# Performance work log

Measured on AMD Instinct MI355X. Metric: run time of the kernel, lower is better.

## Reference

```python
import jax, jax.numpy as jnp
import numpy as np

NPOINT = 10  # hardcoded in Sampler.__init__
INIT_DIST = 1e10  # matches pointnet2 CUDA kernel init


def setup_inputs() -> dict:
    key = jax.random.key(0)
    xyz = jax.random.normal(key, (64, 262144, 3), dtype=jnp.float32)
    return {"xyz": xyz}


def reference(xyz):
    """Furthest point sampling: returns (B, NPOINT) int32 indices,
    same semantics as pointnet2_utils.furthest_point_sample."""
    B, N, _ = xyz.shape
    init_dists = jnp.full((B, N), INIT_DIST, dtype=xyz.dtype)
    init_idx = jnp.zeros((B,), dtype=jnp.int32)  # kernel starts at index 0
    batch = jnp.arange(B)

    def step(carry, _):
        dists, last = carry
        last_pt = xyz[batch, last]                      # (B, 3)
        d = jnp.sum((xyz - last_pt[:, None, :]) ** 2, axis=-1)  # (B, N)
        dists = jnp.minimum(dists, d)
        nxt = jnp.argmax(dists, axis=-1).astype(jnp.int32)
        return (dists, nxt), nxt

    _, rest = jax.lax.scan(step, (init_dists, init_idx), None, length=NPOINT - 1)
    idx = jnp.concatenate([init_idx[None, :], rest], axis=0).T  # (B, NPOINT)
    return idx
```

## Files before the change

### kernel.cpp

```cpp
#include <hip/hip_runtime.h>


#define NPOINT 10
#define NB     64
#define NPTS   262144
#define QN     256
#define QCH    1024
#define TPB    256
#define GB     64
#define INIT_DIST 1e10f

__device__ __forceinline__ float sqdist(float x, float y, float z,
                                        float cx, float cy, float cz) {
    float dx = x - cx, dy = y - cy, dz = z - cz;
    return __fadd_rn(__fadd_rn(__fmul_rn(dx, dx), __fmul_rn(dy, dy)),
                     __fmul_rn(dz, dz));
}

__device__ __forceinline__ unsigned long long packvi(float v, int i) {
    return ((unsigned long long)__float_as_uint(v) << 32) |
           (unsigned)(0xFFFFFFFFu - (unsigned)i);
}
__device__ __forceinline__ int unpack_idx(unsigned long long w) {
    return (int)(0xFFFFFFFFu - (unsigned)(w & 0xFFFFFFFFull));
}

__device__ __forceinline__ void wave_argmax(float& v, int& i) {
    #pragma unroll
    for (int off = 32; off > 0; off >>= 1) {
        float ov = __shfl_down(v, off); int oi = __shfl_down(i, off);
        if (ov > v || (ov == v && oi < i)) { v = ov; i = oi; }
    }
}

__global__ __launch_bounds__(TPB) void fps_scan1(
    const float* __restrict__ xyz, int* __restrict__ out,
    float4* __restrict__ sel,
    float* __restrict__ ub, float* __restrict__ cd, int* __restrict__ ui,
    float* __restrict__ px, float* __restrict__ py, float* __restrict__ pz,
    unsigned long long* __restrict__ win)
{
    const int c = blockIdx.x, b = blockIdx.y, tid = threadIdx.x;
    const int lane = tid & 63, wv = tid >> 6;
    const float* xyzb = xyz + (size_t)b * NPTS * 3;
    const float c0x = xyzb[0], c0y = xyzb[1], c0z = xyzb[2];
    __shared__ float s_v[4];
    __shared__ int   s_i[4];

    const int p0 = c * QCH + tid * 4;
    const float4* src = (const float4*)(xyzb + (size_t)p0 * 3);
    float4 a = src[0], m = src[1], e = src[2];
    float X[4] = {a.x, a.w, m.z, e.y};
    float Y[4] = {a.y, m.x, m.w, e.z};
    float Z[4] = {a.z, m.y, e.x, e.w};
    float bv = -1.0f; int bi = 0;
    #pragma unroll
    for (int j = 0; j < 4; ++j) {
        float d = fminf(INIT_DIST, sqdist(X[j], Y[j], Z[j], c0x, c0y, c0z));
        if (d > bv) { bv = d; bi = p0 + j; }
    }
    wave_argmax(bv, bi);
    if (lane == 0) { s_v[wv] = bv; s_i[wv] = bi; }
    __syncthreads();
    if (tid == 0) {
        float v = s_v[0]; int i = s_i[0];
        #pragma unroll
        for (int w = 1; w < 4; ++w) {
            float ov = s_v[w]; int oi = s_i[w];
            if (ov > v || (ov == v && oi < i)) { v = ov; i = oi; }
        }
        const int o = b * QN + c;
        ub[o] = v; cd[o] = v; ui[o] = i;
        const float* qq = xyzb + (size_t)i * 3;
        px[o] = qq[0]; py[o] = qq[1]; pz[o] = qq[2];
        atomicMax(win + (size_t)1 * NB * 16 + b * 16, packvi(v, i));
        if (c == 0) {
            out[b * NPOINT + 0] = 0;
            sel[b * NPOINT + 0] = make_float4(c0x, c0y, c0z, 0.f);
        }
    }
}

template <int R>
__global__ __launch_bounds__(TPB) void fps_step(
    const float* __restrict__ xyz, int* __restrict__ out,
    float4* __restrict__ sel,
    const float* __restrict__ ub_i, const float* __restrict__ cd_i,
    const int* __restrict__ ui_i, const float* __restrict__ px_i,
    const float* __restrict__ py_i, const float* __restrict__ pz_i,
    float* __restrict__ ub_o, float* __restrict__ cd_o, int* __restrict__ ui_o,
    float* __restrict__ px_o, float* __restrict__ py_o, float* __restrict__ pz_o,
    unsigned long long* __restrict__ win)
{
    const int g = blockIdx.x, b = blockIdx.y, tid = threadIdx.x;
    const int lane = tid & 63, wv = tid >> 6;
    const float* xyzb = xyz + (size_t)b * NPTS * 3;
    const int boff = b * QN;

    __shared__ float scx[NPOINT], scy[NPOINT], scz[NPOINT];
    __shared__ float s_r[4], s_qub[4];
    __shared__ float s_v[4];
    __shared__ int   s_i[4];

    const unsigned long long w = win[(size_t)(R - 1) * NB * 16 + b * 16];
    const int prevIdx = unpack_idx(w);
    const float* pp = xyzb + (size_t)prevIdx * 3;
    const float pcx = pp[0], pcy = pp[1], pcz = pp[2];

    if (tid < R - 1) {
        float4 q = sel[b * NPOINT + tid];
        scx[tid] = q.x; scy[tid] = q.y; scz[tid] = q.z;
    }
    if (tid == 0) { scx[R - 1] = pcx; scy[R - 1] = pcy; scz[R - 1] = pcz; }

    float myub = ub_i[boff + tid];
    float mycd = cd_i[boff + tid];
    int   myui = ui_i[boff + tid];
    float mx = px_i[boff + tid], my = py_i[boff + tid], mz = pz_i[boff + tid];
    mycd = fminf(mycd, sqdist(mx, my, mz, pcx, pcy, pcz));

    float rv = mycd;
    #pragma unroll
    for (int off = 32; off > 0; off >>= 1)
        rv = fmaxf(rv, __shfl_down(rv, off));
    if (lane == 0) s_r[wv] = rv;
    const int dq = tid - 4 * g;
    if (dq >= 0 && dq < 4) s_qub[dq] = myub;
    __syncthreads();
    const float LB = fmaxf(fmaxf(s_r[0], s_r[1]), fmaxf(s_r[2], s_r[3]));

    if (g == 0 && tid == 0) {
        out[b * NPOINT + (R - 1)] = prevIdx;
        sel[b * NPOINT + (R - 1)] = make_float4(pcx, pcy, pcz, 0.f);
    }

    const bool mine = (dq >= 0 && dq < 4);
    const bool my_survives = mine && (myub >= LB);
    if (mine && !my_survives) {
        ub_o[boff + tid] = myub; cd_o[boff + tid] = mycd; ui_o[boff + tid] = myui;
        px_o[boff + tid] = mx;   py_o[boff + tid] = my;   pz_o[boff + tid] = mz;
    }

    unsigned long long* const wr = win + (size_t)R * NB * 16 + b * 16;
    #pragma unroll
    for (int j = 0; j < 4; ++j) {
        if (s_qub[j] < LB) continue;
        const int q = 4 * g + j;
        const int p0 = q * QCH + tid * 4;
        const float4* src = (const float4*)(xyzb + (size_t)p0 * 3);
        float4 a = src[0], m4 = src[1], e = src[2];
        float X[4] = {a.x, a.w, m4.z, e.y};
        float Y[4] = {a.y, m4.x, m4.w, e.z};
        float Z[4] = {a.z, m4.y, e.x, e.w};
        float bv = -1.0f; int bi = 0;
        #pragma unroll
        for (int t = 0; t < 4; ++t) {
            float dmin = INIT_DIST;
            #pragma unroll
            for (int k = 0; k < R; ++k)
                dmin = fminf(dmin, sqdist(X[t], Y[t], Z[t], scx[k], scy[k], scz[k]));
            if (dmin > bv) { bv = dmin; bi = p0 + t; }
        }
        wave_argmax(bv, bi);
        if (lane == 0) { s_v[wv] = bv; s_i[wv] = bi; }
        __syncthreads();
        if (tid == 0) {
            float v = s_v[0]; int i = s_i[0];
            #pragma unroll
            for (int u = 1; u < 4; ++u) {
                float ov = s_v[u]; int oi = s_i[u];
                if (ov > v || (ov == v && oi < i)) { v = ov; i = oi; }
            }
            const float* qq = xyzb + (size_t)i * 3;
            ub_o[boff + q] = v; cd_o[boff + q] = v; ui_o[boff + q] = i;
            px_o[boff + q] = qq[0]; py_o[boff + q] = qq[1]; pz_o[boff + q] = qq[2];
            atomicMax(wr, packvi(v, i));
        }
        __syncthreads();
    }
}

__global__ __launch_bounds__(64) void fps_final(
    const unsigned long long* __restrict__ win, int* __restrict__ out)
{
    const int b = threadIdx.x;
    if (b < NB)
        out[b * NPOINT + (NPOINT - 1)] =
            unpack_idx(win[(size_t)(NPOINT - 1) * NB * 16 + b * 16]);
}

extern "C" void kernel_launch(void* const* d_in, const int* in_sizes, int n_in,
                              void* d_out, int out_size, void* d_ws, size_t ws_size,
                              hipStream_t stream) {
    const float* xyz = (const float*)d_in[0];
    int* out = (int*)d_out;
    char* ws = (char*)d_ws;

    float* ub0 = (float*)(ws + 0);       float* ub1 = (float*)(ws + 65536);
    float* cd0 = (float*)(ws + 131072);  float* cd1 = (float*)(ws + 196608);
    int*   ui0 = (int*)  (ws + 262144);  int*   ui1 = (int*)  (ws + 327680);
    float* px0 = (float*)(ws + 393216);  float* px1 = (float*)(ws + 458752);
    float* py0 = (float*)(ws + 524288);  float* py1 = (float*)(ws + 589824);
    float* pz0 = (float*)(ws + 655360);  float* pz1 = (float*)(ws + 720896);
    float4* sel = (float4*)(ws + 786432);
    unsigned long long* win = (unsigned long long*)(ws + 796672);

    hipMemsetAsync(win, 0, NPOINT * NB * 16 * sizeof(unsigned long long), stream);

    dim3 gridA(QN, NB), gridB(GB, NB), block(TPB);
    fps_scan1<<<gridA, block, 0, stream>>>(xyz, out, sel, ub0, cd0, ui0,
                                           px0, py0, pz0, win);
    fps_step<2><<<gridB, block, 0, stream>>>(xyz, out, sel, ub0, cd0, ui0, px0, py0, pz0,
                                             ub1, cd1, ui1, px1, py1, pz1, win);
    fps_step<3><<<gridB, block, 0, stream>>>(xyz, out, sel, ub1, cd1, ui1, px1, py1, pz1,
                                             ub0, cd0, ui0, px0, py0, pz0, win);
    fps_step<4><<<gridB, block, 0, stream>>>(xyz, out, sel, ub0, cd0, ui0, px0, py0, pz0,
                                             ub1, cd1, ui1, px1, py1, pz1, win);
    fps_step<5><<<gridB, block, 0, stream>>>(xyz, out, sel, ub1, cd1, ui1, px1, py1, pz1,
                                             ub0, cd0, ui0, px0, py0, pz0, win);
    fps_step<6><<<gridB, block, 0, stream>>>(xyz, out, sel, ub0, cd0, ui0, px0, py0, pz0,
                                             ub1, cd1, ui1, px1, py1, pz1, win);
    fps_step<7><<<gridB, block, 0, stream>>>(xyz, out, sel, ub1, cd1, ui1, px1, py1, pz1,
                                             ub0, cd0, ui0, px0, py0, pz0, win);
    fps_step<8><<<gridB, block, 0, stream>>>(xyz, out, sel, ub0, cd0, ui0, px0, py0, pz0,
                                             ub1, cd1, ui1, px1, py1, pz1, win);
    fps_step<9><<<gridB, block, 0, stream>>>(xyz, out, sel, ub1, cd1, ui1, px1, py1, pz1,
                                             ub0, cd0, ui0, px0, py0, pz0, win);
    fps_final<<<dim3(1), dim3(64), 0, stream>>>(win, out);
}
```

Baseline: 192.3 us.

## Refine FPS pruning to per-wave 256-point records with separate bound kernel

Replaces the 256 chunks of 1024 points per batch with 1024 records of 256 points, each scanned by a single wave with no block-level syncs. Each step is split into a small per-batch kernel that updates cached record distances and computes the global lower bound, and a kernel that rescans only records whose upper bound reaches that bound. The finer records are meant to prune more points per step and drop the intra-block barriers, and the memset is folded into the first kernel. The cost is twice as many launches, plus serial per-batch reduction kernels running on only 64 blocks.

New measurement: 304.1 us. 58.1% more time.

```diff
diff --git a/kernel.cpp b/kernel.cpp
--- a/kernel.cpp
+++ b/kernel.cpp
@@ -4,10 +4,9 @@
 #define NPOINT 10
 #define NB     64
 #define NPTS   262144
-#define QN     256
-#define QCH    1024
+#define NR     1024
+#define HCH    256
 #define TPB    256
-#define GB     64
 #define INIT_DIST 1e10f
 
 __device__ __forceinline__ float sqdist(float x, float y, float z,
@@ -33,160 +32,163 @@
     }
 }
 
-__global__ __launch_bounds__(TPB) void fps_scan1(
-    const float* __restrict__ xyz, int* __restrict__ out,
-    float4* __restrict__ sel,
-    float* __restrict__ ub, float* __restrict__ cd, int* __restrict__ ui,
-    float* __restrict__ px, float* __restrict__ py, float* __restrict__ pz,
-    unsigned long long* __restrict__ win)
-{
-    const int c = blockIdx.x, b = blockIdx.y, tid = threadIdx.x;
-    const int lane = tid & 63, wv = tid >> 6;
-    const float* xyzb = xyz + (size_t)b * NPTS * 3;
-    const float c0x = xyzb[0], c0y = xyzb[1], c0z = xyzb[2];
-    __shared__ float s_v[4];
-    __shared__ int   s_i[4];
-
-    const int p0 = c * QCH + tid * 4;
+template <int R>
+__device__ __forceinline__ void scanW(const float* __restrict__ xyzb, int rec,
+                                      int lane, const float* scx,
+                                      const float* scy, const float* scz,
+                                      float& outv, int& outi) {
+    float cx[R], cy[R], cz[R];
+    #pragma unroll
+    for (int k = 0; k < R; ++k) { cx[k] = scx[k]; cy[k] = scy[k]; cz[k] = scz[k]; }
+    const int p0 = rec * HCH + lane * 4;
     const float4* src = (const float4*)(xyzb + (size_t)p0 * 3);
-    float4 a = src[0], m = src[1], e = src[2];
-    float X[4] = {a.x, a.w, m.z, e.y};
-    float Y[4] = {a.y, m.x, m.w, e.z};
-    float Z[4] = {a.z, m.y, e.x, e.w};
+    float4 a = src[0], m4 = src[1], e = src[2];
+    float X[4] = {a.x, a.w, m4.z, e.y};
+    float Y[4] = {a.y, m4.x, m4.w, e.z};
+    float Z[4] = {a.z, m4.y, e.x, e.w};
     float bv = -1.0f; int bi = 0;
     #pragma unroll
     for (int j = 0; j < 4; ++j) {
-        float d = fminf(INIT_DIST, sqdist(X[j], Y[j], Z[j], c0x, c0y, c0z));
-        if (d > bv) { bv = d; bi = p0 + j; }
+        float dmin = INIT_DIST;
+        #pragma unroll
+        for (int k = 0; k < R; ++k)
+            dmin = fminf(dmin, sqdist(X[j], Y[j], Z[j], cx[k], cy[k], cz[k]));
+        if (dmin > bv) { bv = dmin; bi = p0 + j; }
     }
     wave_argmax(bv, bi);
-    if (lane == 0) { s_v[wv] = bv; s_i[wv] = bi; }
-    __syncthreads();
-    if (tid == 0) {
-        float v = s_v[0]; int i = s_i[0];
-        #pragma unroll
-        for (int w = 1; w < 4; ++w) {
-            float ov = s_v[w]; int oi = s_i[w];
-            if (ov > v || (ov == v && oi < i)) { v = ov; i = oi; }
-        }
-        const int o = b * QN + c;
-        ub[o] = v; cd[o] = v; ui[o] = i;
-        const float* qq = xyzb + (size_t)i * 3;
-        px[o] = qq[0]; py[o] = qq[1]; pz[o] = qq[2];
-        atomicMax(win + (size_t)1 * NB * 16 + b * 16, packvi(v, i));
-        if (c == 0) {
-            out[b * NPOINT + 0] = 0;
-            sel[b * NPOINT + 0] = make_float4(c0x, c0y, c0z, 0.f);
-        }
-    }
-}
-
-template <int R>
-__global__ __launch_bounds__(TPB) void fps_step(
-    const float* __restrict__ xyz, int* __restrict__ out,
-    float4* __restrict__ sel,
-    const float* __restrict__ ub_i, const float* __restrict__ cd_i,
-    const int* __restrict__ ui_i, const float* __restrict__ px_i,
-    const float* __restrict__ py_i, const float* __restrict__ pz_i,
-    float* __restrict__ ub_o, float* __restrict__ cd_o, int* __restrict__ ui_o,
-    float* __restrict__ px_o, float* __restrict__ py_o, float* __restrict__ pz_o,
+    outv = bv; outi = bi;
+}
+
+__global__ __launch_bounds__(TPB) void fps_scan1(
+    const float* __restrict__ xyz,
+    float* __restrict__ ub, float* __restrict__ cd, int* __restrict__ ui,
+    float* __restrict__ px, float* __restrict__ py, float* __restrict__ pz,
     unsigned long long* __restrict__ win)
 {
     const int g = blockIdx.x, b = blockIdx.y, tid = threadIdx.x;
     const int lane = tid & 63, wv = tid >> 6;
     const float* xyzb = xyz + (size_t)b * NPTS * 3;
-    const int boff = b * QN;
-
+    if (g == 0 && tid < NPOINT) win[((size_t)tid * NB + b) * 16] = 0ULL;
+
+    const float c0x = xyzb[0], c0y = xyzb[1], c0z = xyzb[2];
+    const int rec = g * 4 + wv;
+    const float ax[1] = {c0x}, ay[1] = {c0y}, az[1] = {c0z};
+    float v; int i;
+    scanW<1>(xyzb, rec, lane, ax, ay, az, v, i);
+    if (lane == 0) {
+        const int o = b * NR + rec;
+        ub[o] = v; cd[o] = v; ui[o] = i;
+        const float* qq = xyzb + (size_t)i * 3;
+        px[o] = qq[0]; py[o] = qq[1]; pz[o] = qq[2];
+    }
+}
+
+template <int R>
+__global__ __launch_bounds__(TPB) void fps_stepA(
+    const float* __restrict__ xyz, int* __restrict__ out,
+    float4* __restrict__ sel,
+    const float* __restrict__ ub, float* __restrict__ cd,
+    const int* __restrict__ ui,
+    const float* __restrict__ px, const float* __restrict__ py,
+    const float* __restrict__ pz,
+    const unsigned long long* __restrict__ win, float* __restrict__ lb)
+{
+    const int b = blockIdx.x, tid = threadIdx.x;
+    const float* xyzb = xyz + (size_t)b * NPTS * 3;
+    __shared__ float s_v[TPB];
+    __shared__ int   s_i[TPB];
+    __shared__ float s_c[3];
+
+    int prevIdx;
+    if constexpr (R == 2) {
+        float v = -1.0f; int i = 0x7fffffff;
+        #pragma unroll
+        for (int t0 = 0; t0 < NR; t0 += TPB) {
+            const int o = b * NR + t0 + tid;
+            float u = ub[o]; int j = ui[o];
+            if (u > v || (u == v && j < i)) { v = u; i = j; }
+        }
+        s_v[tid] = v; s_i[tid] = i;
+        __syncthreads();
+        for (int st = TPB / 2; st > 0; st >>= 1) {
+            if (tid < st) {
+                float ov = s_v[tid + st]; int oi = s_i[tid + st];
+                if (ov > s_v[tid] || (ov == s_v[tid] && oi < s_i[tid])) {
+                    s_v[tid] = ov; s_i[tid] = oi;
+                }
+            }
+            __syncthreads();
+        }
+        prevIdx = s_i[0];
+        if (tid == 0) {
+            out[b * NPOINT + 0] = 0;
+            sel[b * 16 + 0] = make_float4(xyzb[0], xyzb[1], xyzb[2], 0.f);
+        }
+    } else {
+        prevIdx = unpack_idx(win[((size_t)(R - 1) * NB + b) * 16]);
+    }
+
+    if (tid == 0) {
+        out[b * NPOINT + (R - 1)] = prevIdx;
+        const float* pp = xyzb + (size_t)prevIdx * 3;
+        s_c[0] = pp[0]; s_c[1] = pp[1]; s_c[2] = pp[2];
+        if constexpr (R < NPOINT)
+            sel[b * 16 + (R - 1)] = make_float4(pp[0], pp[1], pp[2], 0.f);
+    }
+    __syncthreads();
+
+    if constexpr (R < NPOINT) {
+        const float ccx = s_c[0], ccy = s_c[1], ccz = s_c[2];
+        float m = -1.0f;
+        #pragma unroll
+        for (int t0 = 0; t0 < NR; t0 += TPB) {
+            const int o = b * NR + t0 + tid;
+            float c2 = fminf(cd[o], sqdist(px[o], py[o], pz[o], ccx, ccy, ccz));
+            cd[o] = c2;
+            m = fmaxf(m, c2);
+        }
+        s_v[tid] = m;
+        __syncthreads();
+        for (int st = TPB / 2; st > 0; st >>= 1) {
+            if (tid < st) s_v[tid] = fmaxf(s_v[tid], s_v[tid + st]);
+            __syncthreads();
+        }
+        if (tid == 0) lb[b * 32] = s_v[0];
+    }
+}
+
+template <int R>
+__global__ __launch_bounds__(TPB) void fps_stepB(
+    const float* __restrict__ xyz, const float4* __restrict__ sel,
+    float* __restrict__ ub, float* __restrict__ cd, int* __restrict__ ui,
+    float* __restrict__ px, float* __restrict__ py, float* __restrict__ pz,
+    const float* __restrict__ lb, unsigned long long* __restrict__ win)
+{
+    const int s = blockIdx.x, b = blockIdx.y, tid = threadIdx.x;
+    const int lane = tid & 63, wv = tid >> 6;
+    const float* xyzb = xyz + (size_t)b * NPTS * 3;
     __shared__ float scx[NPOINT], scy[NPOINT], scz[NPOINT];
-    __shared__ float s_r[4], s_qub[4];
-    __shared__ float s_v[4];
-    __shared__ int   s_i[4];
-
-    const unsigned long long w = win[(size_t)(R - 1) * NB * 16 + b * 16];
-    const int prevIdx = unpack_idx(w);
-    const float* pp = xyzb + (size_t)prevIdx * 3;
-    const float pcx = pp[0], pcy = pp[1], pcz = pp[2];
-
-    if (tid < R - 1) {
-        float4 q = sel[b * NPOINT + tid];
+    if (tid < R) {
+        float4 q = sel[b * 16 + tid];
         scx[tid] = q.x; scy[tid] = q.y; scz[tid] = q.z;
     }
-    if (tid == 0) { scx[R - 1] = pcx; scy[R - 1] = pcy; scz[R - 1] = pcz; }
-
-    float myub = ub_i[boff + tid];
-    float mycd = cd_i[boff + tid];
-    int   myui = ui_i[boff + tid];
-    float mx = px_i[boff + tid], my = py_i[boff + tid], mz = pz_i[boff + tid];
-    mycd = fminf(mycd, sqdist(mx, my, mz, pcx, pcy, pcz));
-
-    float rv = mycd;
-    #pragma unroll
-    for (int off = 32; off > 0; off >>= 1)
-        rv = fmaxf(rv, __shfl_down(rv, off));
-    if (lane == 0) s_r[wv] = rv;
-    const int dq = tid - 4 * g;
-    if (dq >= 0 && dq < 4) s_qub[dq] = myub;
     __syncthreads();
-    const float LB = fmaxf(fmaxf(s_r[0], s_r[1]), fmaxf(s_r[2], s_r[3]));
-
-    if (g == 0 && tid == 0) {
-        out[b * NPOINT + (R - 1)] = prevIdx;
-        sel[b * NPOINT + (R - 1)] = make_float4(pcx, pcy, pcz, 0.f);
-    }
-
-    const bool mine = (dq >= 0 && dq < 4);
-    const bool my_survives = mine && (myub >= LB);
-    if (mine && !my_survives) {
-        ub_o[boff + tid] = myub; cd_o[boff + tid] = mycd; ui_o[boff + tid] = myui;
-        px_o[boff + tid] = mx;   py_o[boff + tid] = my;   pz_o[boff + tid] = mz;
-    }
-
-    unsigned long long* const wr = win + (size_t)R * NB * 16 + b * 16;
-    #pragma unroll
-    for (int j = 0; j < 4; ++j) {
-        if (s_qub[j] < LB) continue;
-        const int q = 4 * g + j;
-        const int p0 = q * QCH + tid * 4;
-        const float4* src = (const float4*)(xyzb + (size_t)p0 * 3);
-        float4 a = src[0], m4 = src[1], e = src[2];
-        float X[4] = {a.x, a.w, m4.z, e.y};
-        float Y[4] = {a.y, m4.x, m4.w, e.z};
-        float Z[4] = {a.z, m4.y, e.x, e.w};
-        float bv = -1.0f; int bi = 0;
-        #pragma unroll
-        for (int t = 0; t < 4; ++t) {
-            float dmin = INIT_DIST;
-            #pragma unroll
-            for (int k = 0; k < R; ++k)
-                dmin = fminf(dmin, sqdist(X[t], Y[t], Z[t], scx[k], scy[k], scz[k]));
-            if (dmin > bv) { bv = dmin; bi = p0 + t; }
-        }
-        wave_argmax(bv, bi);
-        if (lane == 0) { s_v[wv] = bv; s_i[wv] = bi; }
-        __syncthreads();
-        if (tid == 0) {
-            float v = s_v[0]; int i = s_i[0];
-            #pragma unroll
-            for (int u = 1; u < 4; ++u) {
-                float ov = s_v[u]; int oi = s_i[u];
-                if (ov > v || (ov == v && oi < i)) { v = ov; i = oi; }
-            }
+    const float LB = lb[b * 32];
+    unsigned long long* const wr = win + ((size_t)R * NB + b) * 16;
+
+    const int r0 = s * 64 + wv * 16;
+    for (int t = 0; t < 16; ++t) {
+        const int rec = r0 + t, o = b * NR + rec;
+        if (ub[o] < LB) continue;
+        float v; int i;
+        scanW<R>(xyzb, rec, lane, scx, scy, scz, v, i);
+        if (lane == 0) {
+            ub[o] = v; cd[o] = v; ui[o] = i;
             const float* qq = xyzb + (size_t)i * 3;
-            ub_o[boff + q] = v; cd_o[boff + q] = v; ui_o[boff + q] = i;
-            px_o[boff + q] = qq[0]; py_o[boff + q] = qq[1]; pz_o[boff + q] = qq[2];
+            px[o] = qq[0]; py[o] = qq[1]; pz[o] = qq[2];
             atomicMax(wr, packvi(v, i));
         }
-        __syncthreads();
-    }
-}
-
-__global__ __launch_bounds__(64) void fps_final(
-    const unsigned long long* __restrict__ win, int* __restrict__ out)
-{
-    const int b = threadIdx.x;
-    if (b < NB)
-        out[b * NPOINT + (NPOINT - 1)] =
-            unpack_idx(win[(size_t)(NPOINT - 1) * NB * 16 + b * 16]);
+    }
 }
 
 extern "C" void kernel_launch(void* const* d_in, const int* in_sizes, int n_in,
@@ -196,35 +198,24 @@
     int* out = (int*)d_out;
     char* ws = (char*)d_ws;
 
-    float* ub0 = (float*)(ws + 0);       float* ub1 = (float*)(ws + 65536);
-    float* cd0 = (float*)(ws + 131072);  float* cd1 = (float*)(ws + 196608);
-    int*   ui0 = (int*)  (ws + 262144);  int*   ui1 = (int*)  (ws + 327680);
-    float* px0 = (float*)(ws + 393216);  float* px1 = (float*)(ws + 458752);
-    float* py0 = (float*)(ws + 524288);  float* py1 = (float*)(ws + 589824);
-    float* pz0 = (float*)(ws + 655360);  float* pz1 = (float*)(ws + 720896);
-    float4* sel = (float4*)(ws + 786432);
-    unsigned long long* win = (unsigned long long*)(ws + 796672);
-
-    hipMemsetAsync(win, 0, NPOINT * NB * 16 * sizeof(unsigned long long), stream);
-
-    dim3 gridA(QN, NB), gridB(GB, NB), block(TPB);
-    fps_scan1<<<gridA, block, 0, stream>>>(xyz, out, sel, ub0, cd0, ui0,
-                                           px0, py0, pz0, win);
-    fps_step<2><<<gridB, block, 0, stream>>>(xyz, out, sel, ub0, cd0, ui0, px0, py0, pz0,
-                                             ub1, cd1, ui1, px1, py1, pz1, win);
-    fps_step<3><<<gridB, block, 0, stream>>>(xyz, out, sel, ub1, cd1, ui1, px1, py1, pz1,
-                                             ub0, cd0, ui0, px0, py0, pz0, win);
-    fps_step<4><<<gridB, block, 0, stream>>>(xyz, out, sel, ub0, cd0, ui0, px0, py0, pz0,
-                                             ub1, cd1, ui1, px1, py1, pz1, win);
-    fps_step<5><<<gridB, block, 0, stream>>>(xyz, out, sel, ub1, cd1, ui1, px1, py1, pz1,
-                                             ub0, cd0, ui0, px0, py0, pz0, win);
-    fps_step<6><<<gridB, block, 0, stream>>>(xyz, out, sel, ub0, cd0, ui0, px0, py0, pz0,
-                                             ub1, cd1, ui1, px1, py1, pz1, win);
-    fps_step<7><<<gridB, block, 0, stream>>>(xyz, out, sel, ub1, cd1, ui1, px1, py1, pz1,
-                                             ub0, cd0, ui0, px0, py0, pz0, win);
-    fps_step<8><<<gridB, block, 0, stream>>>(xyz, out, sel, ub0, cd0, ui0, px0, py0, pz0,
-                                             ub1, cd1, ui1, px1, py1, pz1, win);
-    fps_step<9><<<gridB, block, 0, stream>>>(xyz, out, sel, ub1, cd1, ui1, px1, py1, pz1,
-                                             ub0, cd0, ui0, px0, py0, pz0, win);
-    fps_final<<<dim3(1), dim3(64), 0, stream>>>(win, out);
-}
+    float* ub = (float*)(ws + 0);
+    float* cd = (float*)(ws + (size_t)256 * 1024);
+    int*   ui = (int*)  (ws + (size_t)512 * 1024);
+    float* px = (float*)(ws + (size_t)768 * 1024);
+    float* py = (float*)(ws + (size_t)1024 * 1024);
+    float* pz = (float*)(ws + (size_t)1280 * 1024);
+    float4* sel = (float4*)(ws + (size_t)1536 * 1024);
+    float* lb = (float*)(ws + (size_t)1552 * 1024);
+    unsigned long long* win = (unsigned long long*)(ws + (size_t)1560 * 1024);
+
+    dim3 gA(NR / 4, NB), gB(16, NB), blk(TPB);
+    fps_scan1<<<gA, blk, 0, stream>>>(xyz, ub, cd, ui, px, py, pz, win);
+
+#define STEP(R) \
+    fps_stepA<R><<<dim3(NB), blk, 0, stream>>>(xyz, out, sel, ub, cd, ui, px, py, pz, win, lb); \
+    fps_stepB<R><<<gB, blk, 0, stream>>>(xyz, sel, ub, cd, ui, px, py, pz, lb, win);
+    STEP(2) STEP(3) STEP(4) STEP(5) STEP(6) STEP(7) STEP(8) STEP(9)
+#undef STEP
+    fps_stepA<NPOINT><<<dim3(NB), blk, 0, stream>>>(xyz, out, sel, ub, cd, ui,
+                                                    px, py, pz, win, lb);
+}
```

## Drop memset and final launch; fuse last step into per-batch tail kernel

Applied to the files above, without the earlier changes.

Removes the hipMemsetAsync by having the first scan kernel zero the winner slots it needs. Step 2 now derives its previous index by block-reducing the chunk bounds instead of reading an atomic, so the first-scan atomics go away. The last step plus the final-write kernel are replaced by one kernel with a 1024-thread block per batch that compacts surviving chunks and scans them. This saves two launches, but the tail runs only 64 blocks, which could underuse the GPU if many chunks survive.

New measurement: 288.8 us. 1.5x slower.

```diff
diff --git a/kernel.cpp b/kernel.cpp
--- a/kernel.cpp
+++ b/kernel.cpp
@@ -47,6 +47,9 @@
     __shared__ float s_v[4];
     __shared__ int   s_i[4];
 
+    if (c == 0 && tid >= 2 && tid <= 8)
+        win[((size_t)tid * NB + b) * 16] = 0ULL;
+
     const int p0 = c * QCH + tid * 4;
     const float4* src = (const float4*)(xyzb + (size_t)p0 * 3);
     float4 a = src[0], m = src[1], e = src[2];
@@ -73,7 +76,6 @@
         ub[o] = v; cd[o] = v; ui[o] = i;
         const float* qq = xyzb + (size_t)i * 3;
         px[o] = qq[0]; py[o] = qq[1]; pz[o] = qq[2];
-        atomicMax(win + (size_t)1 * NB * 16 + b * 16, packvi(v, i));
         if (c == 0) {
             out[b * NPOINT + 0] = 0;
             sel[b * NPOINT + 0] = make_float4(c0x, c0y, c0z, 0.f);
@@ -101,22 +103,42 @@
     __shared__ float s_r[4], s_qub[4];
     __shared__ float s_v[4];
     __shared__ int   s_i[4];
-
-    const unsigned long long w = win[(size_t)(R - 1) * NB * 16 + b * 16];
-    const int prevIdx = unpack_idx(w);
-    const float* pp = xyzb + (size_t)prevIdx * 3;
-    const float pcx = pp[0], pcy = pp[1], pcz = pp[2];
-
-    if (tid < R - 1) {
-        float4 q = sel[b * NPOINT + tid];
-        scx[tid] = q.x; scy[tid] = q.y; scz[tid] = q.z;
-    }
-    if (tid == 0) { scx[R - 1] = pcx; scy[R - 1] = pcy; scz[R - 1] = pcz; }
+    __shared__ int   s_prev;
 
     float myub = ub_i[boff + tid];
     float mycd = cd_i[boff + tid];
     int   myui = ui_i[boff + tid];
     float mx = px_i[boff + tid], my = py_i[boff + tid], mz = pz_i[boff + tid];
+
+    int prevIdx;
+    if constexpr (R == 2) {
+        float v = myub; int i = myui;
+        wave_argmax(v, i);
+        if (lane == 0) { s_v[wv] = v; s_i[wv] = i; }
+        __syncthreads();
+        if (tid == 0) {
+            float v2 = s_v[0]; int i2 = s_i[0];
+            #pragma unroll
+            for (int w = 1; w < 4; ++w)
+                if (s_v[w] > v2 || (s_v[w] == v2 && s_i[w] < i2)) {
+                    v2 = s_v[w]; i2 = s_i[w];
+                }
+            s_prev = i2;
+        }
+        __syncthreads();
+        prevIdx = s_prev;
+    } else {
+        prevIdx = unpack_idx(win[((size_t)(R - 1) * NB + b) * 16]);
+    }
+    const float* pp = xyzb + (size_t)prevIdx * 3;
+    const float pcx = pp[0], pcy = pp[1], pcz = pp[2];
+
+    if (tid < R - 1) {
+        float4 q = sel[b * NPOINT + tid];
+        scx[tid] = q.x; scy[tid] = q.y; scz[tid] = q.z;
+    }
+    if (tid == 0) { scx[R - 1] = pcx; scy[R - 1] = pcy; scz[R - 1] = pcz; }
+
     mycd = fminf(mycd, sqdist(mx, my, mz, pcx, pcy, pcz));
 
     float rv = mycd;
@@ -141,7 +163,7 @@
         px_o[boff + tid] = mx;   py_o[boff + tid] = my;   pz_o[boff + tid] = mz;
     }
 
-    unsigned long long* const wr = win + (size_t)R * NB * 16 + b * 16;
+    unsigned long long* const wr = win + ((size_t)R * NB + b) * 16;
     #pragma unroll
     for (int j = 0; j < 4; ++j) {
         if (s_qub[j] < LB) continue;
@@ -180,13 +202,122 @@
     }
 }
 
-__global__ __launch_bounds__(64) void fps_final(
-    const unsigned long long* __restrict__ win, int* __restrict__ out)
+template <int R>
+__device__ __forceinline__ void scanQ(const float* __restrict__ xyzb, int q,
+                                      int lane, const float* scx,
+                                      const float* scy, const float* scz,
+                                      float& outv, int& outi) {
+    float cx[R], cy[R], cz[R];
+    #pragma unroll
+    for (int k = 0; k < R; ++k) { cx[k] = scx[k]; cy[k] = scy[k]; cz[k] = scz[k]; }
+    float bestv = -1.0f; int besti = 0;
+    const int p0 = q * QCH + lane * 16;
+    #pragma unroll
+    for (int grp = 0; grp < 4; ++grp) {
+        const float4* src = (const float4*)(xyzb + (size_t)(p0 + grp * 4) * 3);
+        float4 a = src[0], m4 = src[1], e = src[2];
+        float X[4] = {a.x, a.w, m4.z, e.y};
+        float Y[4] = {a.y, m4.x, m4.w, e.z};
+        float Z[4] = {a.z, m4.y, e.x, e.w};
+        #pragma unroll
+        for (int j = 0; j < 4; ++j) {
+            float dmin = INIT_DIST;
+            #pragma unroll
+            for (int k = 0; k < R; ++k)
+                dmin = fminf(dmin, sqdist(X[j], Y[j], Z[j], cx[k], cy[k], cz[k]));
+            if (dmin > bestv) { bestv = dmin; besti = p0 + grp * 4 + j; }
+        }
+    }
+    wave_argmax(bestv, besti);
+    outv = bestv; outi = besti;
+}
+
+__global__ __launch_bounds__(1024, 1) void fps_tail(
+    const float* __restrict__ xyz, int* __restrict__ out,
+    const float4* __restrict__ sel,
+    const float* __restrict__ ub_i, const float* __restrict__ cd_i,
+    const float* __restrict__ px_i, const float* __restrict__ py_i,
+    const float* __restrict__ pz_i,
+    const unsigned long long* __restrict__ win)
 {
-    const int b = threadIdx.x;
-    if (b < NB)
-        out[b * NPOINT + (NPOINT - 1)] =
-            unpack_idx(win[(size_t)(NPOINT - 1) * NB * 16 + b * 16]);
+    const int b = blockIdx.x, tid = threadIdx.x;
+    const int lane = tid & 63, wv = tid >> 6;
+    const float* xyzb = xyz + (size_t)b * NPTS * 3;
+    const int boff = b * QN;
+
+    __shared__ float scx[9], scy[9], scz[9];
+    __shared__ float s_v[16]; __shared__ int s_i[16];
+    __shared__ int   s_cnt[16], s_pre[16], s_sl[QN], s_M;
+    __shared__ float s_lb;
+
+    if (tid < 8) {
+        float4 q = sel[b * NPOINT + tid];
+        scx[tid] = q.x; scy[tid] = q.y; scz[tid] = q.z;
+    }
+    if (tid == 0) {
+        const int prevIdx = unpack_idx(win[((size_t)8 * NB + b) * 16]);
+        out[b * NPOINT + 8] = prevIdx;
+        const float* pp = xyzb + (size_t)prevIdx * 3;
+        scx[8] = pp[0]; scy[8] = pp[1]; scz[8] = pp[2];
+    }
+    __syncthreads();
+
+    float myub = -1.0f, mycd = -1.0f;
+    if (tid < QN) {
+        myub = ub_i[boff + tid];
+        mycd = fminf(cd_i[boff + tid],
+                     sqdist(px_i[boff + tid], py_i[boff + tid],
+                            pz_i[boff + tid], scx[8], scy[8], scz[8]));
+    }
+    float m = mycd;
+    #pragma unroll
+    for (int off = 32; off > 0; off >>= 1) m = fmaxf(m, __shfl_down(m, off));
+    if (lane == 0) s_v[wv] = m;
+    __syncthreads();
+    if (tid == 0) {
+        float mm = s_v[0];
+        #pragma unroll
+        for (int w = 1; w < 16; ++w) mm = fmaxf(mm, s_v[w]);
+        s_lb = mm;
+    }
+    __syncthreads();
+    const float LB = s_lb;
+
+    const bool flag = (tid < QN) && (myub >= LB);
+    const unsigned long long bm = __ballot(flag);
+    if (lane == 0) s_cnt[wv] = (int)__popcll(bm);
+    __syncthreads();
+    if (tid == 0) {
+        int acc = 0;
+        #pragma unroll
+        for (int w = 0; w < 16; ++w) { s_pre[w] = acc; acc += s_cnt[w]; }
+        s_M = acc;
+    }
+    __syncthreads();
+    if (flag) {
+        int pos = s_pre[wv] + (int)__popcll(bm & ((1ull << lane) - 1ull));
+        s_sl[pos] = tid;
+    }
+    __syncthreads();
+    const int M = s_M;
+
+    float bv = -1.0f; int bi = 0x7fffffff;
+    for (int t = wv; t < M; t += 16) {
+        float v; int i;
+        scanQ<9>(xyzb, s_sl[t], lane, scx, scy, scz, v, i);
+        if (lane == 0 && (v > bv || (v == bv && i < bi))) { bv = v; bi = i; }
+    }
+    if (lane == 0) { s_v[wv] = bv; s_i[wv] = bi; }
+    __syncthreads();
+    if (tid == 0) {
+        float v2 = s_v[0]; int i2 = s_i[0];
+        #pragma unroll
+        for (int w = 1; w < 16; ++w)
+            if (s_v[w] > v2 || (s_v[w] == v2 && s_i[w] < i2)) {
+                v2 = s_v[w]; i2 = s_i[w];
+            }
+        out[b * NPOINT + 9] = i2;
+    }
 }
 
 extern "C" void kernel_launch(void* const* d_in, const int* in_sizes, int n_in,
@@ -203,9 +334,7 @@
     float* py0 = (float*)(ws + 524288);  float* py1 = (float*)(ws + 589824);
     float* pz0 = (float*)(ws + 655360);  float* pz1 = (float*)(ws + 720896);
     float4* sel = (float4*)(ws + 786432);
-    unsigned long long* win = (unsigned long long*)(ws + 796672);
-
-    hipMemsetAsync(win, 0, NPOINT * NB * 16 * sizeof(unsigned long long), stream);
+    unsigned long long* win = (unsigned long long*)(ws + 798720);
 
     dim3 gridA(QN, NB), gridB(GB, NB), block(TPB);
     fps_scan1<<<gridA, block, 0, stream>>>(xyz, out, sel, ub0, cd0, ui0,
@@ -224,7 +353,6 @@
                                              ub0, cd0, ui0, px0, py0, pz0, win);
     fps_step<8><<<gridB, block, 0, stream>>>(xyz, out, sel, ub0, cd0, ui0, px0, py0, pz0,
                                              ub1, cd1, ui1, px1, py1, pz1, win);
-    fps_step<9><<<gridB, block, 0, stream>>>(xyz, out, sel, ub1, cd1, ui1, px1, py1, pz1,
-                                             ub0, cd0, ui0, px0, py0, pz0, win);
-    fps_final<<<dim3(1), dim3(64), 0, stream>>>(win, out);
-}
+    fps_tail<<<dim3(NB), dim3(1024), 0, stream>>>(xyz, out, sel, ub1, cd1,
+                                                  px1, py1, pz1, win);
+}
```
